# Performance work log

Hardware: AMD Instinct MI355X
Metric: run time of the kernel (lower is better)

The kernel has to match this reference:

```python
import jax, jax.numpy as jnp
import numpy as np

N = 20000       # nodes
DIN = 256       # in_channels
DOUT = 256      # out_channels (per head)
H = 8           # num_heads
K_CURV = 1.0    # Lorentz manifold curvature k
POWER_K = 2.0   # args.power_k
EPS = 1e-6


def setup_inputs() -> dict:
    key = jax.random.key(0)
    ks = jax.random.split(key, 10)
    s = 1.0 / np.sqrt(DIN)
    return {
        "query_input": jax.random.normal(ks[0], (N, DIN), dtype=jnp.float32),
        "source_input": jax.random.normal(ks[1], (N, DIN), dtype=jnp.float32),
        # per-head HypLinear weights (stacked over heads)
        "Wq_w": jax.random.normal(ks[2], (H, DOUT, DIN), dtype=jnp.float32) * s,
        "Wq_b": jax.random.normal(ks[3], (H, DOUT), dtype=jnp.float32) * 0.01,
        "Wk_w": jax.random.normal(ks[4], (H, DOUT, DIN), dtype=jnp.float32) * s,
        "Wk_b": jax.random.normal(ks[5], (H, DOUT), dtype=jnp.float32) * 0.01,
        "Wv_w": jax.random.normal(ks[6], (H, DOUT, DIN), dtype=jnp.float32) * s,
        "Wv_b": jax.random.normal(ks[7], (H, DOUT), dtype=jnp.float32) * 0.01,
        "norm_scale": jnp.ones((), dtype=jnp.float32),
        "vmap_w": jax.random.normal(ks[8], (DOUT, DIN), dtype=jnp.float32) * s,
        "vmap_b": jax.random.normal(ks[9], (DOUT,), dtype=jnp.float32) * 0.01,
    }


def _fp(x, p):
    # torch: norm(x,2,-1,keepdim) / norm(x**p,2,-1,keepdim) * x**p
    xp = x ** p
    norm_x = jnp.sqrt(jnp.sum(x * x, axis=-1, keepdims=True))
    norm_xp = jnp.sqrt(jnp.sum(xp * xp, axis=-1, keepdims=True))
    return norm_x / norm_xp * xp


def reference(query_input, source_input, Wq_w, Wq_b, Wk_w, Wk_b, Wv_w, Wv_b,
              norm_scale, vmap_w, vmap_b):
    # Per-head HypLinear space components; the Lorentz time component that
    # HypLinear prepends is sliced off ([..., 1:]) by linear_focus_attention,
    # so only the space part (the plain linear output) is needed here.
    qs = jnp.einsum('nd,hod->nho', query_input, Wq_w) + Wq_b   # [N,H,DOUT]
    ks = jnp.einsum('nd,hod->nho', source_input, Wk_w) + Wk_b  # [N,H,DOUT]
    v = jnp.einsum('nd,hod->nho', source_input, Wv_w) + Wv_b   # [N,H,DOUT]

    inv_ns = 1.0 / jnp.abs(norm_scale)
    phi_q = _fp((jax.nn.relu(qs) + EPS) * inv_ns, POWER_K)
    phi_k = _fp((jax.nn.relu(ks) + EPS) * inv_ns, POWER_K)

    # O(N) kernelized attention: summarize keys/values per head
    ktv = jnp.einsum('nhm,nhd->hmd', phi_k, v)                  # [H,DOUT,DOUT]
    numerator = jnp.einsum('nhm,hmd->nhd', phi_q, ktv)          # [N,H,DOUT]
    k_sum = jnp.sum(phi_k, axis=0)                              # [H,DOUT]
    denominator = jnp.einsum('nhd,hd->nh', phi_q, k_sum)[..., None]
    attn_output = numerator / (denominator + EPS)

    vss = jnp.einsum('nhd,od->nho', v, vmap_w) + vmap_b         # v_map_mlp(v)
    attn_output = attn_output + vss

    # trans_heads_concat = False -> mean over heads
    out_space = jnp.mean(attn_output, axis=1)                   # [N,DOUT]
    out_time = jnp.sqrt(jnp.sum(out_space ** 2, axis=-1, keepdims=True) + K_CURV)
    return jnp.concatenate([out_time, out_space], axis=-1)      # [N,DOUT+1]
```

## Files before the change

kernel.cpp:

```cpp
#include <hip/hip_runtime.h>
#include <hip/hip_bf16.h>

#define N_NODES 20000
#define NH      8
#define NG      16
#define G2      1250
#define FEPS    1e-6f
#define XS_LD   264
#define TL      72
#define P3R     80

typedef __attribute__((ext_vector_type(8))) short bf16x8;
typedef __attribute__((ext_vector_type(4))) float f32x4;
typedef unsigned short u16;

__device__ __forceinline__ float bf2f(u16 u) {
    union { unsigned int i; float f; } v; v.i = ((unsigned int)u) << 16; return v.f;
}
__device__ __forceinline__ u16 f2bf(float f) {
    union { float f; unsigned int i; } v; v.f = f;
    return (u16)((v.i + 0x7fffu + ((v.i >> 16) & 1u)) >> 16);
}
__device__ __forceinline__ int pk2(float a, float b) {
    return (int)f2bf(a) | ((int)f2bf(b) << 16);
}
__device__ __forceinline__ int4 cvt8(const float* __restrict__ s) {
    float4 a = *(const float4*)s;
    float4 b = *(const float4*)(s + 4);
    int4 w;
    w.x = pk2(a.x, a.y); w.y = pk2(a.z, a.w);
    w.z = pk2(b.x, b.y); w.w = pk2(b.z, b.w);
    return w;
}

__global__ __launch_bounds__(256) void wprep_kernel(
    const float* __restrict__ Wq, const float* __restrict__ Wk, const float* __restrict__ Wv,
    u16* __restrict__ Wqb, u16* __restrict__ Wkb, u16* __restrict__ Wvb,
    float* __restrict__ Wsum)
{
    const int z = blockIdx.y;
    if (z < 3) {
        const float* s = (z == 0) ? Wq : (z == 1) ? Wk : Wv;
        u16* d = (z == 0) ? Wqb : (z == 1) ? Wkb : Wvb;
        int i = blockIdx.x * 256 + threadIdx.x;
        float4 v = reinterpret_cast<const float4*>(s)[i];
        ushort4 o;
        o.x = f2bf(v.x); o.y = f2bf(v.y); o.z = f2bf(v.z); o.w = f2bf(v.w);
        reinterpret_cast<ushort4*>(d)[i] = o;
    } else {
        if (blockIdx.x >= 256) return;
        int i = blockIdx.x * 256 + threadIdx.x;
        float s = 0.f;
#pragma unroll
        for (int h = 0; h < NH; ++h) s += Wv[(size_t)h * 65536 + i];
        Wsum[i] = s;
    }
}

__global__ __launch_bounds__(256) void wfin_kernel(
    const float* __restrict__ Wsum, const float* __restrict__ vmap_w,
    const float* __restrict__ bv, const float* __restrict__ vmap_b,
    u16* __restrict__ Wavg, float* __restrict__ bavg)
{
    const int o = blockIdx.x, t = threadIdx.x;
    __shared__ float buf[256];
    if (o < 256) {
        buf[t] = vmap_w[(size_t)o * 256 + t];
        __syncthreads();
        float acc = 0.f;
#pragma unroll 4
        for (int e = 0; e < 256; ++e)
            acc += buf[e] * Wsum[(size_t)e * 256 + t];
        Wavg[(size_t)o * 256 + t] = f2bf(acc * 0.125f);
    } else {
        float s = 0.f;
        for (int h = 0; h < NH; ++h) s += bv[h * 256 + t];
        buf[t] = s * 0.125f;
        __syncthreads();
        float acc = vmap_b[t];
        for (int e = 0; e < 256; ++e) acc += vmap_w[(size_t)t * 256 + e] * buf[e];
        bavg[t] = acc;
    }
}

__global__ __launch_bounds__(512, 2) void pass2_kernel(
    const float* __restrict__ srcf,
    const u16* __restrict__ Wkb, const float* __restrict__ bk,
    const u16* __restrict__ Wvb, const float* __restrict__ bv,
    const float* __restrict__ ns_ptr,
    u16* __restrict__ P,
    float* __restrict__ ksum)
{
    const int bid = blockIdx.x;
    const int h = bid & 7, gr = bid >> 3, g = gr % NG, dh = gr / NG;
    const int t = threadIdx.x;
    const int lane = t & 63, wid = t >> 6;
    const int r16 = lane & 15, kgrp = lane >> 4;

    __shared__ char smem[75008];
    u16* Xs = (u16*)smem;
    u16* VT = (u16*)smem;
    u16* KT = (u16*)(smem + 33792);
    float* red = (float*)(smem + 70656);
    float* scl = (float*)(smem + 74752);

    const float inv_ns = 1.0f / fabsf(ns_ptr[0]);
    const u16* Wkh = Wkb + (size_t)h * 65536;
    const u16* Wvh = Wvb + (size_t)h * 65536;

    const int n0g = g * G2;
    const int rlim = min(G2, N_NODES - n0g);
    const int nt = (rlim + 63) >> 6;

    f32x4 kacc[2][8];
#pragma unroll
    for (int i = 0; i < 2; ++i)
#pragma unroll
        for (int j = 0; j < 8; ++j) kacc[i][j] = (f32x4){0.f, 0.f, 0.f, 0.f};
    float ksr = 0.f;

    for (int it = 0; it < nt; ++it) {
        const int ln0 = it * 64;
        __syncthreads();
#pragma unroll
        for (int p = 0; p < 4; ++p) {
            int id = p * 512 + t;
            int row = id >> 5, col = (id & 31) * 8;
            int4 w = {0, 0, 0, 0};
            if (ln0 + row < rlim)
                w = cvt8(srcf + ((size_t)(n0g + ln0 + row) * 256 + col));
            *(int4*)&Xs[row * XS_LD + col] = w;
        }
        __syncthreads();

        f32x4 acc2[2][4];
#pragma unroll
        for (int i = 0; i < 2; ++i)
#pragma unroll
            for (int j = 0; j < 4; ++j) acc2[i][j] = (f32x4){0.f, 0.f, 0.f, 0.f};
#pragma unroll
        for (int kc = 0; kc < 4; ++kc) {
#pragma unroll
            for (int kk = 0; kk < 2; ++kk) {
                bf16x8 a[2];
#pragma unroll
                for (int i = 0; i < 2; ++i)
                    a[i] = *(const bf16x8*)&Wkh[(size_t)(wid * 32 + i * 16 + r16) * 256 + kc * 64 + kk * 32 + kgrp * 8];
#pragma unroll
                for (int j = 0; j < 4; ++j) {
                    bf16x8 b = *(const bf16x8*)&Xs[(j * 16 + r16) * XS_LD + kc * 64 + kk * 32 + kgrp * 8];
#pragma unroll
                    for (int i = 0; i < 2; ++i)
                        acc2[i][j] = __builtin_amdgcn_mfma_f32_16x16x32_bf16(a[i], b, acc2[i][j], 0, 0, 0);
                }
            }
        }
#pragma unroll
        for (int i = 0; i < 2; ++i) {
#pragma unroll
            for (int j = 0; j < 4; ++j) {
                int n = j * 16 + r16;
#pragma unroll
                for (int r = 0; r < 4; ++r) {
                    int m = wid * 32 + i * 16 + kgrp * 4 + r;
                    float x = acc2[i][j][r] + bk[h * 256 + m];
                    x = (fmaxf(x, 0.f) + FEPS) * inv_ns;
                    KT[m * TL + n] = f2bf(x);
                }
            }
        }
        __syncthreads();
        {
            int c = t & 63, ch = t >> 6;
            float s1 = 0.f, s2 = 0.f;
#pragma unroll
            for (int i = 0; i < 32; ++i) {
                float x = bf2f(KT[(ch * 32 + i) * TL + c]);
                float q = x * x;
                s1 += q; s2 += q * q;
            }
            red[ch * 64 + c] = s1;
            red[512 + ch * 64 + c] = s2;
        }
        __syncthreads();
        if (t < 64) {
            float s1 = 0.f, s2 = 0.f;
#pragma unroll
            for (int ch = 0; ch < 8; ++ch) {
                s1 += red[ch * 64 + t];
                s2 += red[512 + ch * 64 + t];
            }
            scl[t] = (ln0 + t < rlim) ? sqrtf(s1) / sqrtf(s2) : 0.f;
        }
        __syncthreads();
        {
            const int m = t >> 1, q0 = (t & 1) * 32;
            float kp = 0.f;
#pragma unroll
            for (int j = 0; j < 4; ++j) {
                bf16x8 v8 = *(const bf16x8*)&KT[m * TL + q0 + j * 8];
                bf16x8 w8;
#pragma unroll
                for (int jj = 0; jj < 8; ++jj) {
                    float x = bf2f((u16)v8[jj]);
                    float ph = x * x * scl[q0 + j * 8 + jj];
                    u16 pb = f2bf(ph);
                    w8[jj] = (short)pb;
                    kp += bf2f(pb);
                }
                *(bf16x8*)&KT[m * TL + q0 + j * 8] = w8;
            }
            ksr += kp;
        }
        f32x4 accv[4];
#pragma unroll
        for (int j = 0; j < 4; ++j) accv[j] = (f32x4){0.f, 0.f, 0.f, 0.f};
#pragma unroll
        for (int kc = 0; kc < 4; ++kc) {
#pragma unroll
            for (int kk = 0; kk < 2; ++kk) {
                bf16x8 a = *(const bf16x8*)&Wvh[(size_t)(dh * 128 + wid * 16 + r16) * 256 + kc * 64 + kk * 32 + kgrp * 8];
#pragma unroll
                for (int j = 0; j < 4; ++j) {
                    bf16x8 b = *(const bf16x8*)&Xs[(j * 16 + r16) * XS_LD + kc * 64 + kk * 32 + kgrp * 8];
                    accv[j] = __builtin_amdgcn_mfma_f32_16x16x32_bf16(a, b, accv[j], 0, 0, 0);
                }
            }
        }
        __syncthreads();
#pragma unroll
        for (int j = 0; j < 4; ++j) {
            int n = j * 16 + r16;
#pragma unroll
            for (int r = 0; r < 4; ++r) {
                int dl = wid * 16 + kgrp * 4 + r;
                VT[dl * TL + n] = f2bf(accv[j][r] + bv[h * 256 + dh * 128 + dl]);
            }
        }
        __syncthreads();
#pragma unroll
        for (int kk = 0; kk < 2; ++kk) {
            bf16x8 a[2];
#pragma unroll
            for (int i = 0; i < 2; ++i)
                a[i] = *(const bf16x8*)&KT[(wid * 32 + i * 16 + r16) * TL + kk * 32 + kgrp * 8];
#pragma unroll
            for (int j = 0; j < 8; ++j) {
                bf16x8 b = *(const bf16x8*)&VT[(j * 16 + r16) * TL + kk * 32 + kgrp * 8];
#pragma unroll
                for (int i = 0; i < 2; ++i)
                    kacc[i][j] = __builtin_amdgcn_mfma_f32_16x16x32_bf16(a[i], b, kacc[i][j], 0, 0, 0);
            }
        }
    }
    {
        u16* Pb = P + (size_t)bid * 32768;
#pragma unroll
        for (int i = 0; i < 2; ++i) {
#pragma unroll
            for (int j = 0; j < 8; ++j) {
                int dl = j * 16 + r16;
                int m0 = wid * 32 + i * 16 + kgrp * 4;
                ushort4 o;
                o.x = f2bf(kacc[i][j][0]); o.y = f2bf(kacc[i][j][1]);
                o.z = f2bf(kacc[i][j][2]); o.w = f2bf(kacc[i][j][3]);
                *(ushort4*)&Pb[dl * 256 + m0] = o;
            }
        }
    }
    if (dh == 0) atomicAdd(&ksum[h * 256 + (t >> 1)], ksr);
}

__global__ __launch_bounds__(256) void ktvreduce_kernel(const u16* __restrict__ P, u16* __restrict__ ktvb)
{
    int idx = blockIdx.x * 256 + threadIdx.x;
    int m4 = idx & 63, dl = (idx >> 6) & 127, dh = (idx >> 13) & 1, h = idx >> 14;
    float s0 = 0.f, s1 = 0.f, s2 = 0.f, s3 = 0.f;
#pragma unroll 4
    for (int g = 0; g < NG; ++g) {
        const u16* Pb = P + (size_t)(h + 8 * (g + NG * dh)) * 32768;
        ushort4 v = *(const ushort4*)&Pb[dl * 256 + m4 * 4];
        s0 += bf2f(v.x); s1 += bf2f(v.y); s2 += bf2f(v.z); s3 += bf2f(v.w);
    }
    ushort4 o;
    o.x = f2bf(s0); o.y = f2bf(s1); o.z = f2bf(s2); o.w = f2bf(s3);
    *(ushort4*)&ktvb[(size_t)h * 65536 + (size_t)(dh * 128 + dl) * 256 + m4 * 4] = o;
}

__global__ __launch_bounds__(512, 1) void pass3_kernel(
    const float* __restrict__ qf, const float* __restrict__ sf,
    const u16* __restrict__ Wqb, const float* __restrict__ bq,
    const float* __restrict__ ns_ptr, const u16* __restrict__ ktvb, const float* __restrict__ ksum,
    const u16* __restrict__ Wavg, const float* __restrict__ bavg, float* __restrict__ out)
{
    const int n0 = blockIdx.x * P3R;
    const int t = threadIdx.x;
    const int lane = t & 63, wid = t >> 6;
    const int r16 = lane & 15, kgrp = lane >> 4;
    const int C0 = wid * 32;

    __shared__ char smem[86016];
    u16* Xs = (u16*)smem;
    u16* Qs = (u16*)(smem + 42240);
    float* ksl = (float*)(smem + 84480);
    float* den = (float*)(smem + 85504);
    float* outs = (float*)smem;

    const float inv_ns = 1.0f / fabsf(ns_ptr[0]);

#pragma unroll
    for (int p = 0; p < 5; ++p) {
        int id = p * 512 + t;
        int row = id >> 5, col = (id & 31) * 8;
        *(int4*)&Xs[row * XS_LD + col] = cvt8(qf + ((size_t)(n0 + row) * 256 + col));
    }
    __syncthreads();

    f32x4 oacc[5][2];
#pragma unroll
    for (int f = 0; f < 5; ++f)
#pragma unroll
        for (int j = 0; j < 2; ++j) oacc[f][j] = (f32x4){0.f, 0.f, 0.f, 0.f};

    for (int h = 0; h < NH; ++h) {
        if (t < 256) ksl[t] = ksum[h * 256 + t];
        f32x4 acc[5][2];
#pragma unroll
        for (int f = 0; f < 5; ++f)
#pragma unroll
            for (int j = 0; j < 2; ++j) acc[f][j] = (f32x4){0.f, 0.f, 0.f, 0.f};
#pragma unroll
        for (int kc = 0; kc < 4; ++kc) {
#pragma unroll
            for (int kk = 0; kk < 2; ++kk) {
                bf16x8 a[5], b[2];
#pragma unroll
                for (int f = 0; f < 5; ++f)
                    a[f] = *(const bf16x8*)&Xs[(f * 16 + r16) * XS_LD + kc * 64 + kk * 32 + kgrp * 8];
#pragma unroll
                for (int j = 0; j < 2; ++j)
                    b[j] = *(const bf16x8*)&Wqb[(size_t)h * 65536 +
                        (size_t)(C0 + j * 16 + r16) * 256 + kc * 64 + kk * 32 + kgrp * 8];
#pragma unroll
                for (int f = 0; f < 5; ++f)
#pragma unroll
                    for (int j = 0; j < 2; ++j)
                        acc[f][j] = __builtin_amdgcn_mfma_f32_16x16x32_bf16(a[f], b[j], acc[f][j], 0, 0, 0);
            }
        }
        __syncthreads();
#pragma unroll
        for (int f = 0; f < 5; ++f) {
#pragma unroll
            for (int j = 0; j < 2; ++j) {
                int c = C0 + j * 16 + r16;
#pragma unroll
                for (int r = 0; r < 4; ++r) {
                    int n = f * 16 + kgrp * 4 + r;
                    float x = acc[f][j][r] + bq[h * 256 + c];
                    x = (fmaxf(x, 0.f) + FEPS) * inv_ns;
                    Qs[n * XS_LD + c] = f2bf(x);
                }
            }
        }
        __syncthreads();
#pragma unroll
        for (int rp = 0; rp < 2; ++rp) {
            int row = rp * 64 + (t >> 3);
            if (row < P3R) {
                int q = t & 7;
                float s1 = 0.f, s2 = 0.f;
                bf16x8 v8s[4];
#pragma unroll
                for (int j = 0; j < 4; ++j) {
                    v8s[j] = *(const bf16x8*)&Qs[row * XS_LD + q * 32 + j * 8];
#pragma unroll
                    for (int jj = 0; jj < 8; ++jj) {
                        float x = bf2f((u16)v8s[j][jj]);
                        float qq = x * x;
                        s1 += qq; s2 += qq * qq;
                    }
                }
                s1 += __shfl_xor(s1, 1, 64); s1 += __shfl_xor(s1, 2, 64); s1 += __shfl_xor(s1, 4, 64);
                s2 += __shfl_xor(s2, 1, 64); s2 += __shfl_xor(s2, 2, 64); s2 += __shfl_xor(s2, 4, 64);
                float sc = sqrtf(s1) / sqrtf(s2);
                float dp = 0.f;
#pragma unroll
                for (int j = 0; j < 4; ++j) {
                    bf16x8 w8;
#pragma unroll
                    for (int jj = 0; jj < 8; ++jj) {
                        float x = bf2f((u16)v8s[j][jj]);
                        float ph = x * x * sc;
                        u16 pb = f2bf(ph);
                        w8[jj] = (short)pb;
                        dp += bf2f(pb) * ksl[q * 32 + j * 8 + jj];
                    }
                    *(bf16x8*)&Qs[row * XS_LD + q * 32 + j * 8] = w8;
                }
                dp += __shfl_xor(dp, 1, 64); dp += __shfl_xor(dp, 2, 64); dp += __shfl_xor(dp, 4, 64);
                if (q == 0) den[row] = 0.125f / (dp + FEPS);
            }
        }
        __syncthreads();
#pragma unroll
        for (int f = 0; f < 5; ++f)
#pragma unroll
            for (int j = 0; j < 2; ++j) acc[f][j] = (f32x4){0.f, 0.f, 0.f, 0.f};
#pragma unroll
        for (int kc = 0; kc < 4; ++kc) {
#pragma unroll
            for (int kk = 0; kk < 2; ++kk) {
                bf16x8 a[5], b[2];
#pragma unroll
                for (int f = 0; f < 5; ++f)
                    a[f] = *(const bf16x8*)&Qs[(f * 16 + r16) * XS_LD + kc * 64 + kk * 32 + kgrp * 8];
#pragma unroll
                for (int j = 0; j < 2; ++j)
                    b[j] = *(const bf16x8*)&ktvb[(size_t)h * 65536 +
                        (size_t)(C0 + j * 16 + r16) * 256 + kc * 64 + kk * 32 + kgrp * 8];
#pragma unroll
                for (int f = 0; f < 5; ++f)
#pragma unroll
                    for (int j = 0; j < 2; ++j)
                        acc[f][j] = __builtin_amdgcn_mfma_f32_16x16x32_bf16(a[f], b[j], acc[f][j], 0, 0, 0);
            }
        }
#pragma unroll
        for (int f = 0; f < 5; ++f) {
#pragma unroll
            for (int r = 0; r < 4; ++r) {
                float dr = den[f * 16 + kgrp * 4 + r];
#pragma unroll
                for (int j = 0; j < 2; ++j)
                    oacc[f][j][r] += acc[f][j][r] * dr;
            }
        }
    }
    __syncthreads();
#pragma unroll
    for (int p = 0; p < 5; ++p) {
        int id = p * 512 + t;
        int row = id >> 5, col = (id & 31) * 8;
        *(int4*)&Qs[row * XS_LD + col] = cvt8(sf + ((size_t)(n0 + row) * 256 + col));
    }
    __syncthreads();
    f32x4 vacc[5][2];
#pragma unroll
    for (int f = 0; f < 5; ++f)
#pragma unroll
        for (int j = 0; j < 2; ++j) vacc[f][j] = (f32x4){0.f, 0.f, 0.f, 0.f};
#pragma unroll
    for (int kc = 0; kc < 4; ++kc) {
#pragma unroll
        for (int kk = 0; kk < 2; ++kk) {
            bf16x8 a[5], b[2];
#pragma unroll
            for (int f = 0; f < 5; ++f)
                a[f] = *(const bf16x8*)&Qs[(f * 16 + r16) * XS_LD + kc * 64 + kk * 32 + kgrp * 8];
#pragma unroll
            for (int j = 0; j < 2; ++j)
                b[j] = *(const bf16x8*)&Wavg[(size_t)(C0 + j * 16 + r16) * 256 + kc * 64 + kk * 32 + kgrp * 8];
#pragma unroll
            for (int f = 0; f < 5; ++f)
#pragma unroll
                for (int j = 0; j < 2; ++j)
                    vacc[f][j] = __builtin_amdgcn_mfma_f32_16x16x32_bf16(a[f], b[j], vacc[f][j], 0, 0, 0);
        }
    }
    __syncthreads();
#pragma unroll
    for (int f = 0; f < 5; ++f) {
#pragma unroll
        for (int j = 0; j < 2; ++j) {
            int c = C0 + j * 16 + r16;
            float bo = bavg[c];
#pragma unroll
            for (int r = 0; r < 4; ++r) {
                int n = f * 16 + kgrp * 4 + r;
                outs[n * 256 + c] = oacc[f][j][r] + vacc[f][j][r] + bo;
            }
        }
    }
    __syncthreads();
#pragma unroll
    for (int rp = 0; rp < 2; ++rp) {
        int row = rp * 64 + (t >> 3);
        if (row < P3R) {
            int q = t & 7;
            float s = 0.f;
#pragma unroll
            for (int c4 = 0; c4 < 8; ++c4) {
                float4 v = *(const float4*)&outs[row * 256 + q * 32 + c4 * 4];
                s += v.x * v.x + v.y * v.y + v.z * v.z + v.w * v.w;
            }
            s += __shfl_xor(s, 1, 64); s += __shfl_xor(s, 2, 64); s += __shfl_xor(s, 4, 64);
            if (q == 0)
                out[(size_t)(n0 + row) * 257] = sqrtf(s + 1.0f);
        }
    }
    {
        int col = t & 255, half = t >> 8;
        for (int rr = 0; rr < 40; ++rr) {
            int row = half * 40 + rr;
            out[(size_t)(n0 + row) * 257 + 1 + col] = outs[row * 256 + col];
        }
    }
}

extern "C" void kernel_launch(void* const* d_in, const int* in_sizes, int n_in,
                              void* d_out, int out_size, void* d_ws, size_t ws_size,
                              hipStream_t stream)
{
    const float* query  = (const float*)d_in[0];
    const float* source = (const float*)d_in[1];
    const float* Wq_w   = (const float*)d_in[2];
    const float* Wq_b   = (const float*)d_in[3];
    const float* Wk_w   = (const float*)d_in[4];
    const float* Wk_b   = (const float*)d_in[5];
    const float* Wv_w   = (const float*)d_in[6];
    const float* Wv_b   = (const float*)d_in[7];
    const float* ns     = (const float*)d_in[8];
    const float* vmap_w = (const float*)d_in[9];
    const float* vmap_b = (const float*)d_in[10];
    float* out = (float*)d_out;

    char* ws = (char*)d_ws;
    size_t off = 0;
    auto alloc = [&](size_t bytes) -> char* {
        char* p = ws + off;
        off += (bytes + 255) & ~(size_t)255;
        return p;
    };
    float* ksum = (float*)alloc((size_t)NH * 256 * 4);
    u16*   Wqb  = (u16*)alloc((size_t)NH * 65536 * 2);
    u16*   Wkb  = (u16*)alloc((size_t)NH * 65536 * 2);
    u16*   Wvb  = (u16*)alloc((size_t)NH * 65536 * 2);
    float* Wsum = (float*)alloc((size_t)65536 * 4);
    u16*   Wavg = (u16*)alloc((size_t)65536 * 2);
    float* bavg = (float*)alloc((size_t)256 * 4);
    u16*   ktvb = (u16*)alloc((size_t)NH * 65536 * 2);

    if (off > ws_size) {
        hipMemsetAsync(d_out, 0x7f, (size_t)out_size * 4, stream);
        return;
    }

    u16* P = (u16*)d_out;

    hipMemsetAsync(ksum, 0, (size_t)NH * 256 * 4, stream);

    wprep_kernel<<<dim3(512, 4), 256, 0, stream>>>(Wq_w, Wk_w, Wv_w, Wqb, Wkb, Wvb, Wsum);
    wfin_kernel<<<257, 256, 0, stream>>>(Wsum, vmap_w, Wv_b, vmap_b, Wavg, bavg);

    pass2_kernel<<<16 * NG, 512, 0, stream>>>(source, Wkb, Wk_b, Wvb, Wv_b, ns, P, ksum);
    ktvreduce_kernel<<<512, 256, 0, stream>>>(P, ktvb);
    pass3_kernel<<<250, 512, 0, stream>>>(query, source, Wqb, Wq_b, ns, ktvb, ksum, Wavg, bavg, out);
}
```

Baseline: 314.4 us.

## Prefetch next source tile into registers and fuse key feature-map normalization in registers

The pass2 kernel now prefetches the next 64-row fp32 source tile into registers while the current tile is computed, which hides global-load latency. The per-column norm sums are computed directly from the MFMA accumulators using cross-lane shuffles, removing one LDS round trip and one barrier. The phi_k values are written to LDS once, and the k_sum partials are shuffle-reduced before the atomics. Launch bounds drop to one block per SIMD group, which allows more registers per thread but may reduce occupancy.

```diff
diff --git a/kernel.cpp b/kernel.cpp
--- a/kernel.cpp
+++ b/kernel.cpp
@@ -83,7 +83,7 @@
     }
 }
 
-__global__ __launch_bounds__(512, 2) void pass2_kernel(
+__global__ __launch_bounds__(512, 1) void pass2_kernel(
     const float* __restrict__ srcf,
     const u16* __restrict__ Wkb, const float* __restrict__ bk,
     const u16* __restrict__ Wvb, const float* __restrict__ bv,
@@ -117,7 +117,21 @@
     for (int i = 0; i < 2; ++i)
 #pragma unroll
         for (int j = 0; j < 8; ++j) kacc[i][j] = (f32x4){0.f, 0.f, 0.f, 0.f};
-    float ksr = 0.f;
+    float ksm[8] = {0.f, 0.f, 0.f, 0.f, 0.f, 0.f, 0.f, 0.f};
+
+    float4 pf[8];
+#pragma unroll
+    for (int p = 0; p < 4; ++p) {
+        int id = p * 512 + t;
+        int row = id >> 5, col = (id & 31) * 8;
+        pf[2 * p] = (float4){0.f, 0.f, 0.f, 0.f};
+        pf[2 * p + 1] = (float4){0.f, 0.f, 0.f, 0.f};
+        if (row < rlim) {
+            const float* s = srcf + ((size_t)(n0g + row) * 256 + col);
+            pf[2 * p] = *(const float4*)s;
+            pf[2 * p + 1] = *(const float4*)(s + 4);
+        }
+    }
 
     for (int it = 0; it < nt; ++it) {
         const int ln0 = it * 64;
@@ -126,10 +140,27 @@
         for (int p = 0; p < 4; ++p) {
             int id = p * 512 + t;
             int row = id >> 5, col = (id & 31) * 8;
-            int4 w = {0, 0, 0, 0};
-            if (ln0 + row < rlim)
-                w = cvt8(srcf + ((size_t)(n0g + ln0 + row) * 256 + col));
+            int4 w;
+            w.x = pk2(pf[2 * p].x, pf[2 * p].y);
+            w.y = pk2(pf[2 * p].z, pf[2 * p].w);
+            w.z = pk2(pf[2 * p + 1].x, pf[2 * p + 1].y);
+            w.w = pk2(pf[2 * p + 1].z, pf[2 * p + 1].w);
             *(int4*)&Xs[row * XS_LD + col] = w;
+        }
+        if (it + 1 < nt) {
+            const int ln1 = (it + 1) * 64;
+#pragma unroll
+            for (int p = 0; p < 4; ++p) {
+                int id = p * 512 + t;
+                int row = id >> 5, col = (id & 31) * 8;
+                pf[2 * p] = (float4){0.f, 0.f, 0.f, 0.f};
+                pf[2 * p + 1] = (float4){0.f, 0.f, 0.f, 0.f};
+                if (ln1 + row < rlim) {
+                    const float* s = srcf + ((size_t)(n0g + ln1 + row) * 256 + col);
+                    pf[2 * p] = *(const float4*)s;
+                    pf[2 * p + 1] = *(const float4*)(s + 4);
+                }
+            }
         }
         __syncthreads();
 
@@ -155,62 +186,63 @@
                 }
             }
         }
+        float s1j[4], s2j[4];
+#pragma unroll
+        for (int j = 0; j < 4; ++j) { s1j[j] = 0.f; s2j[j] = 0.f; }
 #pragma unroll
         for (int i = 0; i < 2; ++i) {
 #pragma unroll
             for (int j = 0; j < 4; ++j) {
-                int n = j * 16 + r16;
 #pragma unroll
                 for (int r = 0; r < 4; ++r) {
                     int m = wid * 32 + i * 16 + kgrp * 4 + r;
                     float x = acc2[i][j][r] + bk[h * 256 + m];
                     x = (fmaxf(x, 0.f) + FEPS) * inv_ns;
-                    KT[m * TL + n] = f2bf(x);
-                }
-            }
-        }
-        __syncthreads();
-        {
-            int c = t & 63, ch = t >> 6;
-            float s1 = 0.f, s2 = 0.f;
-#pragma unroll
-            for (int i = 0; i < 32; ++i) {
-                float x = bf2f(KT[(ch * 32 + i) * TL + c]);
-                float q = x * x;
-                s1 += q; s2 += q * q;
-            }
-            red[ch * 64 + c] = s1;
-            red[512 + ch * 64 + c] = s2;
+                    acc2[i][j][r] = x;
+                    float q = x * x;
+                    s1j[j] += q; s2j[j] += q * q;
+                }
+            }
+        }
+#pragma unroll
+        for (int j = 0; j < 4; ++j) {
+            s1j[j] += __shfl_xor(s1j[j], 16, 64); s1j[j] += __shfl_xor(s1j[j], 32, 64);
+            s2j[j] += __shfl_xor(s2j[j], 16, 64); s2j[j] += __shfl_xor(s2j[j], 32, 64);
+        }
+        if (kgrp == 0) {
+#pragma unroll
+            for (int j = 0; j < 4; ++j) {
+                int n = j * 16 + r16;
+                red[n * 8 + wid] = s1j[j];
+                red[512 + n * 8 + wid] = s2j[j];
+            }
         }
         __syncthreads();
         if (t < 64) {
             float s1 = 0.f, s2 = 0.f;
 #pragma unroll
-            for (int ch = 0; ch < 8; ++ch) {
-                s1 += red[ch * 64 + t];
-                s2 += red[512 + ch * 64 + t];
+            for (int w8 = 0; w8 < 8; ++w8) {
+                s1 += red[t * 8 + w8];
+                s2 += red[512 + t * 8 + w8];
             }
             scl[t] = (ln0 + t < rlim) ? sqrtf(s1) / sqrtf(s2) : 0.f;
         }
         __syncthreads();
-        {
-            const int m = t >> 1, q0 = (t & 1) * 32;
-            float kp = 0.f;
-#pragma unroll
-            for (int j = 0; j < 4; ++j) {
-                bf16x8 v8 = *(const bf16x8*)&KT[m * TL + q0 + j * 8];
-                bf16x8 w8;
-#pragma unroll
-                for (int jj = 0; jj < 8; ++jj) {
-                    float x = bf2f((u16)v8[jj]);
-                    float ph = x * x * scl[q0 + j * 8 + jj];
-                    u16 pb = f2bf(ph);
-                    w8[jj] = (short)pb;
-                    kp += bf2f(pb);
-                }
-                *(bf16x8*)&KT[m * TL + q0 + j * 8] = w8;
-            }
-            ksr += kp;
+#pragma unroll
+        for (int j = 0; j < 4; ++j) {
+            int n = j * 16 + r16;
+            float sc = scl[n];
+#pragma unroll
+            for (int i = 0; i < 2; ++i) {
+#pragma unroll
+                for (int r = 0; r < 4; ++r) {
+                    int m = wid * 32 + i * 16 + kgrp * 4 + r;
+                    float x = acc2[i][j][r];
+                    u16 pb = f2bf(x * x * sc);
+                    KT[m * TL + n] = pb;
+                    ksm[i * 4 + r] += bf2f(pb);
+                }
+            }
         }
         f32x4 accv[4];
 #pragma unroll
@@ -268,7 +300,19 @@
             }
         }
     }
-    if (dh == 0) atomicAdd(&ksum[h * 256 + (t >> 1)], ksr);
+    if (dh == 0) {
+#pragma unroll
+        for (int i = 0; i < 2; ++i) {
+#pragma unroll
+            for (int r = 0; r < 4; ++r) {
+                float v = ksm[i * 4 + r];
+                v += __shfl_xor(v, 1, 64); v += __shfl_xor(v, 2, 64);
+                v += __shfl_xor(v, 4, 64); v += __shfl_xor(v, 8, 64);
+                if (r16 == 0)
+                    atomicAdd(&ksum[h * 256 + wid * 32 + i * 16 + kgrp * 4 + r], v);
+            }
+        }
+    }
 }
 
 __global__ __launch_bounds__(256) void ktvreduce_kernel(const u16* __restrict__ P, u16* __restrict__ ktvb)
```

After: 437.0 us. +39.0%, slower.

## Double pass2 block to 1024 threads, splitting MFMA work across 16 waves

Applied to the files above, without the earlier changes.

The key/value summary kernel moves from 512 to 1024 threads per block. Each of the 16 waves now owns 16 rows of the K projection and KTV accumulator, and the V projection is split over d-rows and node halves. The aim is more waves in flight to hide latency and shorter per-wave MFMA chains, with fewer accumulator registers per thread. In exchange it adds more threads per barrier, slightly more LDS for the reduction buffer, and a shuffle reduction before the ksum atomics. Launch bounds of (1024,4) may not be satisfiable given the LDS per block.

```diff
diff --git a/kernel.cpp b/kernel.cpp
--- a/kernel.cpp
+++ b/kernel.cpp
@@ -83,7 +83,7 @@
     }
 }
 
-__global__ __launch_bounds__(512, 2) void pass2_kernel(
+__global__ __launch_bounds__(1024, 4) void pass2_kernel(
     const float* __restrict__ srcf,
     const u16* __restrict__ Wkb, const float* __restrict__ bk,
     const u16* __restrict__ Wvb, const float* __restrict__ bv,
@@ -97,12 +97,12 @@
     const int lane = t & 63, wid = t >> 6;
     const int r16 = lane & 15, kgrp = lane >> 4;
 
-    __shared__ char smem[75008];
+    __shared__ char smem[79104];
     u16* Xs = (u16*)smem;
     u16* VT = (u16*)smem;
     u16* KT = (u16*)(smem + 33792);
     float* red = (float*)(smem + 70656);
-    float* scl = (float*)(smem + 74752);
+    float* scl = (float*)(smem + 78848);
 
     const float inv_ns = 1.0f / fabsf(ns_ptr[0]);
     const u16* Wkh = Wkb + (size_t)h * 65536;
@@ -112,19 +112,19 @@
     const int rlim = min(G2, N_NODES - n0g);
     const int nt = (rlim + 63) >> 6;
 
-    f32x4 kacc[2][8];
-#pragma unroll
-    for (int i = 0; i < 2; ++i)
-#pragma unroll
-        for (int j = 0; j < 8; ++j) kacc[i][j] = (f32x4){0.f, 0.f, 0.f, 0.f};
+    const int vd = (wid & 7) * 16, vn = (wid >> 3) * 32;
+
+    f32x4 kacc[8];
+#pragma unroll
+    for (int j = 0; j < 8; ++j) kacc[j] = (f32x4){0.f, 0.f, 0.f, 0.f};
     float ksr = 0.f;
 
     for (int it = 0; it < nt; ++it) {
         const int ln0 = it * 64;
         __syncthreads();
 #pragma unroll
-        for (int p = 0; p < 4; ++p) {
-            int id = p * 512 + t;
+        for (int p = 0; p < 2; ++p) {
+            int id = p * 1024 + t;
             int row = id >> 5, col = (id & 31) * 8;
             int4 w = {0, 0, 0, 0};
             if (ln0 + row < rlim)
@@ -133,40 +133,30 @@
         }
         __syncthreads();
 
-        f32x4 acc2[2][4];
-#pragma unroll
-        for (int i = 0; i < 2; ++i)
-#pragma unroll
-            for (int j = 0; j < 4; ++j) acc2[i][j] = (f32x4){0.f, 0.f, 0.f, 0.f};
+        f32x4 acc2[4];
+#pragma unroll
+        for (int j = 0; j < 4; ++j) acc2[j] = (f32x4){0.f, 0.f, 0.f, 0.f};
 #pragma unroll
         for (int kc = 0; kc < 4; ++kc) {
 #pragma unroll
             for (int kk = 0; kk < 2; ++kk) {
-                bf16x8 a[2];
-#pragma unroll
-                for (int i = 0; i < 2; ++i)
-                    a[i] = *(const bf16x8*)&Wkh[(size_t)(wid * 32 + i * 16 + r16) * 256 + kc * 64 + kk * 32 + kgrp * 8];
+                bf16x8 a = *(const bf16x8*)&Wkh[(size_t)(wid * 16 + r16) * 256 + kc * 64 + kk * 32 + kgrp * 8];
 #pragma unroll
                 for (int j = 0; j < 4; ++j) {
                     bf16x8 b = *(const bf16x8*)&Xs[(j * 16 + r16) * XS_LD + kc * 64 + kk * 32 + kgrp * 8];
-#pragma unroll
-                    for (int i = 0; i < 2; ++i)
-                        acc2[i][j] = __builtin_amdgcn_mfma_f32_16x16x32_bf16(a[i], b, acc2[i][j], 0, 0, 0);
+                    acc2[j] = __builtin_amdgcn_mfma_f32_16x16x32_bf16(a, b, acc2[j], 0, 0, 0);
                 }
             }
         }
 #pragma unroll
-        for (int i = 0; i < 2; ++i) {
-#pragma unroll
-            for (int j = 0; j < 4; ++j) {
-                int n = j * 16 + r16;
-#pragma unroll
-                for (int r = 0; r < 4; ++r) {
-                    int m = wid * 32 + i * 16 + kgrp * 4 + r;
-                    float x = acc2[i][j][r] + bk[h * 256 + m];
-                    x = (fmaxf(x, 0.f) + FEPS) * inv_ns;
-                    KT[m * TL + n] = f2bf(x);
-                }
+        for (int j = 0; j < 4; ++j) {
+            int n = j * 16 + r16;
+#pragma unroll
+            for (int r = 0; r < 4; ++r) {
+                int m = wid * 16 + kgrp * 4 + r;
+                float x = acc2[j][r] + bk[h * 256 + m];
+                x = (fmaxf(x, 0.f) + FEPS) * inv_ns;
+                KT[m * TL + n] = f2bf(x);
             }
         }
         __syncthreads();
@@ -174,30 +164,30 @@
             int c = t & 63, ch = t >> 6;
             float s1 = 0.f, s2 = 0.f;
 #pragma unroll
-            for (int i = 0; i < 32; ++i) {
-                float x = bf2f(KT[(ch * 32 + i) * TL + c]);
+            for (int i = 0; i < 16; ++i) {
+                float x = bf2f(KT[(ch * 16 + i) * TL + c]);
                 float q = x * x;
                 s1 += q; s2 += q * q;
             }
             red[ch * 64 + c] = s1;
-            red[512 + ch * 64 + c] = s2;
+            red[1024 + ch * 64 + c] = s2;
         }
         __syncthreads();
         if (t < 64) {
             float s1 = 0.f, s2 = 0.f;
 #pragma unroll
-            for (int ch = 0; ch < 8; ++ch) {
+            for (int ch = 0; ch < 16; ++ch) {
                 s1 += red[ch * 64 + t];
-                s2 += red[512 + ch * 64 + t];
+                s2 += red[1024 + ch * 64 + t];
             }
             scl[t] = (ln0 + t < rlim) ? sqrtf(s1) / sqrtf(s2) : 0.f;
         }
         __syncthreads();
         {
-            const int m = t >> 1, q0 = (t & 1) * 32;
+            const int m = t >> 2, q0 = (t & 3) * 16;
             float kp = 0.f;
 #pragma unroll
-            for (int j = 0; j < 4; ++j) {
+            for (int j = 0; j < 2; ++j) {
                 bf16x8 v8 = *(const bf16x8*)&KT[m * TL + q0 + j * 8];
                 bf16x8 w8;
 #pragma unroll
@@ -212,63 +202,60 @@
             }
             ksr += kp;
         }
-        f32x4 accv[4];
-#pragma unroll
-        for (int j = 0; j < 4; ++j) accv[j] = (f32x4){0.f, 0.f, 0.f, 0.f};
+        f32x4 accv[2];
+#pragma unroll
+        for (int j = 0; j < 2; ++j) accv[j] = (f32x4){0.f, 0.f, 0.f, 0.f};
 #pragma unroll
         for (int kc = 0; kc < 4; ++kc) {
 #pragma unroll
             for (int kk = 0; kk < 2; ++kk) {
-                bf16x8 a = *(const bf16x8*)&Wvh[(size_t)(dh * 128 + wid * 16 + r16) * 256 + kc * 64 + kk * 32 + kgrp * 8];
-#pragma unroll
-                for (int j = 0; j < 4; ++j) {
-                    bf16x8 b = *(const bf16x8*)&Xs[(j * 16 + r16) * XS_LD + kc * 64 + kk * 32 + kgrp * 8];
+                bf16x8 a = *(const bf16x8*)&Wvh[(size_t)(dh * 128 + vd + r16) * 256 + kc * 64 + kk * 32 + kgrp * 8];
+#pragma unroll
+                for (int j = 0; j < 2; ++j) {
+                    bf16x8 b = *(const bf16x8*)&Xs[(vn + j * 16 + r16) * XS_LD + kc * 64 + kk * 32 + kgrp * 8];
                     accv[j] = __builtin_amdgcn_mfma_f32_16x16x32_bf16(a, b, accv[j], 0, 0, 0);
                 }
             }
         }
         __syncthreads();
 #pragma unroll
-        for (int j = 0; j < 4; ++j) {
-            int n = j * 16 + r16;
+        for (int j = 0; j < 2; ++j) {
+            int n = vn + j * 16 + r16;
 #pragma unroll
             for (int r = 0; r < 4; ++r) {
-                int dl = wid * 16 + kgrp * 4 + r;
+                int dl = vd + kgrp * 4 + r;
                 VT[dl * TL + n] = f2bf(accv[j][r] + bv[h * 256 + dh * 128 + dl]);
             }
         }
         __syncthreads();
 #pragma unroll
         for (int kk = 0; kk < 2; ++kk) {
-            bf16x8 a[2];
-#pragma unroll
-            for (int i = 0; i < 2; ++i)
-                a[i] = *(const bf16x8*)&KT[(wid * 32 + i * 16 + r16) * TL + kk * 32 + kgrp * 8];
+            bf16x8 a = *(const bf16x8*)&KT[(wid * 16 + r16) * TL + kk * 32 + kgrp * 8];
 #pragma unroll
             for (int j = 0; j < 8; ++j) {
                 bf16x8 b = *(const bf16x8*)&VT[(j * 16 + r16) * TL + kk * 32 + kgrp * 8];
-#pragma unroll
-                for (int i = 0; i < 2; ++i)
-                    kacc[i][j] = __builtin_amdgcn_mfma_f32_16x16x32_bf16(a[i], b, kacc[i][j], 0, 0, 0);
+                kacc[j] = __builtin_amdgcn_mfma_f32_16x16x32_bf16(a, b, kacc[j], 0, 0, 0);
             }
         }
     }
     {
         u16* Pb = P + (size_t)bid * 32768;
 #pragma unroll
-        for (int i = 0; i < 2; ++i) {
-#pragma unroll
-            for (int j = 0; j < 8; ++j) {
-                int dl = j * 16 + r16;
-                int m0 = wid * 32 + i * 16 + kgrp * 4;
-                ushort4 o;
-                o.x = f2bf(kacc[i][j][0]); o.y = f2bf(kacc[i][j][1]);
-                o.z = f2bf(kacc[i][j][2]); o.w = f2bf(kacc[i][j][3]);
-                *(ushort4*)&Pb[dl * 256 + m0] = o;
-            }
-        }
-    }
-    if (dh == 0) atomicAdd(&ksum[h * 256 + (t >> 1)], ksr);
+        for (int j = 0; j < 8; ++j) {
+            int dl = j * 16 + r16;
+            int m0 = wid * 16 + kgrp * 4;
+            ushort4 o;
+            o.x = f2bf(kacc[j][0]); o.y = f2bf(kacc[j][1]);
+            o.z = f2bf(kacc[j][2]); o.w = f2bf(kacc[j][3]);
+            *(ushort4*)&Pb[dl * 256 + m0] = o;
+        }
+    }
+    if (dh == 0) {
+        float v = ksr;
+        v += __shfl_xor(v, 1, 64); v += __shfl_xor(v, 2, 64);
+        if ((lane & 3) == 0)
+            atomicAdd(&ksum[h * 256 + (t >> 2)], v);
+    }
 }
 
 __global__ __launch_bounds__(256) void ktvreduce_kernel(const u16* __restrict__ P, u16* __restrict__ ktvb)
@@ -553,7 +540,7 @@
     wprep_kernel<<<dim3(512, 4), 256, 0, stream>>>(Wq_w, Wk_w, Wv_w, Wqb, Wkb, Wvb, Wsum);
     wfin_kernel<<<257, 256, 0, stream>>>(Wsum, vmap_w, Wv_b, vmap_b, Wavg, bavg);
 
-    pass2_kernel<<<16 * NG, 512, 0, stream>>>(source, Wkb, Wk_b, Wvb, Wv_b, ns, P, ksum);
+    pass2_kernel<<<256, 1024, 0, stream>>>(source, Wkb, Wk_b, Wvb, Wv_b, ns, P, ksum);
     ktvreduce_kernel<<<512, 256, 0, stream>>>(P, ktvb);
     pass3_kernel<<<250, 512, 0, stream>>>(query, source, Wqb, Wq_b, ns, ktvb, ksum, Wavg, bavg, out);
 }
```

Measured after the change: 336.5 us. 1.07x slower.
